# Kernel optimization log

Measured on AMD Instinct MI355X. Metric: run time of the kernel, lower is better.

## Reference

```python
import jax, jax.numpy as jnp
import numpy as np

B, C, T, H, W = 4, 128, 16, 56, 56
NH = 4            # num_heads
HD = C // NH      # head_dim = 32
WT, WH, WW = 4, 7, 7
HID = 4 * C       # mlp hidden
EPS_BN = 1e-5
EPS_LN = 1e-5


def setup_inputs() -> dict:
    key = jax.random.key(0)
    ks = jax.random.split(key, 12)
    s = 0.02
    return {
        "x": jax.random.normal(ks[0], (B, C, T, H, W), dtype=jnp.float32),
        "bn_gamma": jnp.ones((C,), jnp.float32),
        "bn_beta": jnp.zeros((C,), jnp.float32),
        "bn_mean": jax.random.normal(ks[1], (C,), jnp.float32) * 0.1,
        "bn_var": jax.random.uniform(ks[2], (C,), jnp.float32, 0.5, 1.5),
        "qkv_w": jax.random.normal(ks[3], (C, 3 * C), jnp.float32) * s,
        "qkv_b": jnp.zeros((3 * C,), jnp.float32),
        "proj_w": jax.random.normal(ks[4], (C, C), jnp.float32) * s,
        "proj_b": jnp.zeros((C,), jnp.float32),
        "ln_gamma": jnp.ones((C,), jnp.float32),
        "ln_beta": jnp.zeros((C,), jnp.float32),
        "fc1_w": jax.random.normal(ks[5], (C, HID), jnp.float32) * s,
        "fc1_b": jnp.zeros((HID,), jnp.float32),
        "fc2_w": jax.random.normal(ks[6], (HID, C), jnp.float32) * s,
        "fc2_b": jnp.zeros((C,), jnp.float32),
    }


def _window_partition(x):
    # x: (B, C, T, H, W) -> (B*nW, N, C)
    nT, nH, nW = T // WT, H // WH, W // WW
    x = jnp.transpose(x, (0, 2, 3, 4, 1))  # B,T,H,W,C
    x = x.reshape(B, nT, WT, nH, WH, nW, WW, C)
    x = jnp.transpose(x, (0, 1, 3, 5, 2, 4, 6, 7))
    return x.reshape(-1, WT * WH * WW, C)


def _window_reverse(w):
    # w: (B*nW, N, C) -> (B, C, T, H, W)
    nT, nH, nW = T // WT, H // WH, W // WW
    x = w.reshape(B, nT, nH, nW, WT, WH, WW, C)
    x = jnp.transpose(x, (0, 1, 4, 2, 5, 3, 6, 7))
    x = x.reshape(B, T, H, W, C)
    return jnp.transpose(x, (0, 4, 1, 2, 3))


def _forward(x, bn_gamma, bn_beta, bn_mean, bn_var, qkv_w, qkv_b,
             proj_w, proj_b, ln_gamma, ln_beta, fc1_w, fc1_b, fc2_w, fc2_b):
    # --- BN3d (eval mode, running stats) over channel dim ---
    inv = jax.lax.rsqrt(bn_var + EPS_BN)
    bshape = (1, C, 1, 1, 1)
    xn = (x - bn_mean.reshape(bshape)) * (inv * bn_gamma).reshape(bshape) + bn_beta.reshape(bshape)

    # --- windowed MHSA ---
    win = _window_partition(xn)                 # (Bw, N, C)
    Bw, N, _ = win.shape
    qkv = win @ qkv_w + qkv_b                   # (Bw, N, 3C)
    qkv = qkv.reshape(Bw, N, 3, NH, HD)
    q, k, v = [jnp.transpose(qkv[:, :, i], (0, 2, 1, 3)) for i in range(3)]  # (Bw, NH, N, HD)
    scale = 1.0 / np.sqrt(HD).astype(np.float32)
    logits = jnp.einsum('bhnd,bhmd->bhnm', q, k) * scale
    attn = jax.nn.softmax(logits, axis=-1)
    out = jnp.einsum('bhnm,bhmd->bhnd', attn, v)
    out = jnp.transpose(out, (0, 2, 1, 3)).reshape(Bw, N, C)
    out = out @ proj_w + proj_b
    x = x + _window_reverse(out)                # residual

    # --- FFN with LayerNorm on flattened sequence ---
    flat = jnp.transpose(x, (0, 2, 3, 4, 1)).reshape(B, T * H * W, C)
    mu = jnp.mean(flat, axis=-1, keepdims=True)
    var = jnp.var(flat, axis=-1, keepdims=True)
    f = (flat - mu) * jax.lax.rsqrt(var + EPS_LN) * ln_gamma + ln_beta
    f = jax.nn.gelu(f @ fc1_w + fc1_b, approximate=False) @ fc2_w + fc2_b
    flat = flat + f
    return jnp.transpose(flat.reshape(B, T, H, W, C), (0, 4, 1, 2, 3))


def reference(x, bn_gamma, bn_beta, bn_mean, bn_var, qkv_w, qkv_b,
              proj_w, proj_b, ln_gamma, ln_beta, fc1_w, fc1_b, fc2_w, fc2_b):
    return _forward(x, bn_gamma, bn_beta, bn_mean, bn_var, qkv_w, qkv_b,
                    proj_w, proj_b, ln_gamma, ln_beta, fc1_w, fc1_b, fc2_w, fc2_b)
```

## Files before the change

kernel.cpp:

```cpp
#include <hip/hip_runtime.h>
#include <hip/hip_bf16.h>
#include <math.h>


typedef __hip_bfloat16 bf16;
typedef __attribute__((ext_vector_type(8))) short short8;
typedef __attribute__((ext_vector_type(4))) short bhalf4;
typedef __attribute__((ext_vector_type(4))) float f32x4;

__device__ __forceinline__ float b2f(bf16 v) { return __bfloat162float(v); }
__device__ __forceinline__ bf16  f2b(float v) { return __float2bfloat16(v); }

__device__ __forceinline__ float gelu_f(float v) {
    float u = v * 0.70710678118654752f;
    float a = fabsf(u);
    float t = __builtin_amdgcn_rcpf(fmaf(0.3275911f, a, 1.0f));
    float poly = t * fmaf(t, fmaf(t, fmaf(t, fmaf(t, 1.061405429f, -1.453152027f),
                                          1.421413741f), -0.284496736f), 0.254829592f);
    float E = poly * __expf(-a * a);
    float w = (u >= 0.f) ? (2.0f - E) : E;
    return 0.5f * v * w;
}

__global__ __launch_bounds__(256) void k0_prep(
    const float* __restrict__ qkv_w, const float* __restrict__ proj_w,
    const float* __restrict__ w1, const float* __restrict__ w2,
    bf16* __restrict__ qkv_wt, bf16* __restrict__ proj_wt,
    bf16* __restrict__ w1t, bf16* __restrict__ w2t)
{
    int stride = gridDim.x * 256;
    int t0 = blockIdx.x * 256 + threadIdx.x;
    for (int i = t0; i < 384 * 128; i += stride) {
        int j = i >> 7, c = i & 127;
        qkv_wt[i] = f2b(qkv_w[c * 384 + j]);
    }
    for (int i = t0; i < 128 * 128; i += stride) {
        int j = i >> 7, c = i & 127;
        proj_wt[i] = f2b(proj_w[c * 128 + j]);
    }
    for (int i = t0; i < 512 * 128; i += stride) {
        int j = i >> 7, c = i & 127;
        w1t[i] = f2b(w1[c * 512 + j]);
    }
    for (int i = t0; i < 128 * 512; i += stride) {
        int c = i >> 9, j = i & 511;
        w2t[i] = f2b(w2[j * 128 + c]);
    }
}

__global__ __launch_bounds__(256) void k12_bn_qkv(
    const float* __restrict__ x, const float* __restrict__ gamma, const float* __restrict__ beta,
    const float* __restrict__ mean, const float* __restrict__ var,
    const bf16* __restrict__ qkv_wt, const float* __restrict__ qkv_b,
    bf16* __restrict__ Q, bf16* __restrict__ K, bf16* __restrict__ V, int bw0)
{
    __shared__ __align__(16) bf16 sXn[208][136];
    __shared__ __align__(16) bf16 sB[64][136];
    __shared__ float sAc[128], sBc[128];
    int lbw = blockIdx.x;
    int gbw = bw0 + lbw;
    int b   = gbw >> 8;
    int wid = gbw & 255;
    int t0 = (wid >> 6) * 4;
    int h0 = ((wid >> 3) & 7) * 7;
    int w0 = (wid & 7) * 7;
    int tid = threadIdx.x;
    if (tid < 128) {
        float a = gamma[tid] * rsqrtf(var[tid] + 1e-5f);
        sAc[tid] = a;
        sBc[tid] = beta[tid] - mean[tid] * a;
    }
    __syncthreads();
    for (int idx = tid; idx < 128 * 196; idx += 256) {
        int c = idx / 196;
        int n = idx - c * 196;
        int wt = n / 49; int rem = n - wt * 49;
        int wh = rem / 7; int ww = rem - wh * 7;
        int gi = (((b * 128 + c) * 16 + (t0 + wt)) * 56 + (h0 + wh)) * 56 + (w0 + ww);
        sXn[n][c] = f2b(x[gi] * sAc[c] + sBc[c]);
    }
    for (int idx = tid; idx < 12 * 16; idx += 256) {
        int row = 196 + (idx >> 4); int c8 = (idx & 15) * 8;
        *(short8*)&sXn[row][c8] = (short8){0, 0, 0, 0, 0, 0, 0, 0};
    }
    int w = tid >> 6, lane = tid & 63;
    int quad = lane >> 4, l16 = lane & 15;
    const f32x4 zero4 = {0.f, 0.f, 0.f, 0.f};
    for (int jc = 0; jc < 6; ++jc) {
        __syncthreads();
        for (int idx = tid; idx < 1024; idx += 256) {
            int j = idx >> 4; int c8 = (idx & 15) * 8;
            *(short8*)&sB[j][c8] = *(const short8*)&qkv_wt[(long)(jc * 64 + j) * 128 + c8];
        }
        __syncthreads();
        bf16* outw = (jc < 2) ? Q : (jc < 4 ? K : V);
        int jb = (jc & 1) * 64;
        for (int mt = w; mt < 13; mt += 4) {
            f32x4 acc[4];
            #pragma unroll
            for (int nt = 0; nt < 4; ++nt) acc[nt] = zero4;
            #pragma unroll
            for (int kk = 0; kk < 4; ++kk) {
                short8 af = *(const short8*)&sXn[mt * 16 + l16][kk * 32 + quad * 8];
                #pragma unroll
                for (int nt = 0; nt < 4; ++nt) {
                    short8 bfq = *(const short8*)&sB[nt * 16 + l16][kk * 32 + quad * 8];
                    acc[nt] = __builtin_amdgcn_mfma_f32_16x16x32_bf16(af, bfq, acc[nt], 0, 0, 0);
                }
            }
            #pragma unroll
            for (int nt = 0; nt < 4; ++nt) {
                int jcol = jb + nt * 16 + l16;
                int h = jcol >> 5, d = jcol & 31;
                float bias = qkv_b[jc * 64 + nt * 16 + l16];
                bf16* base = outw + ((long)(lbw * 4 + h) * 196) * 32 + d;
                #pragma unroll
                for (int r = 0; r < 4; ++r) {
                    int n = mt * 16 + quad * 4 + r;
                    if (n < 196) base[(long)n * 32] = f2b(acc[nt][r] + bias);
                }
            }
        }
    }
}

__global__ __launch_bounds__(256) void k3_attn(
    const bf16* __restrict__ Q, const bf16* __restrict__ K, const bf16* __restrict__ V,
    bf16* __restrict__ attn_out)
{
    __shared__ __align__(16) bf16 sQ[208][36];
    __shared__ __align__(16) bf16 sK[224][40];
    __shared__ __align__(16) bf16 sVt[32][232];
    __shared__ __align__(16) bf16 sP[4][16][36];
    int bh = blockIdx.x;
    int bw = bh >> 2; int h = bh & 3;
    int tid = threadIdx.x;
    const bf16* qp = Q + (long)bh * 6272;
    const bf16* kp = K + (long)bh * 6272;
    const bf16* vp = V + (long)bh * 6272;
    short8 z8 = {0, 0, 0, 0, 0, 0, 0, 0};
    bhalf4 z4 = {0, 0, 0, 0};
    for (int idx = tid; idx < 784; idx += 256) {
        int row = idx >> 2; int c8 = (idx & 3) * 8;
        short8 qv = *(const short8*)&qp[idx * 8];
        bhalf4 qlo = {qv[0], qv[1], qv[2], qv[3]};
        bhalf4 qhi = {qv[4], qv[5], qv[6], qv[7]};
        *(bhalf4*)&sQ[row][c8]     = qlo;
        *(bhalf4*)&sQ[row][c8 + 4] = qhi;
        *(short8*)&sK[row][c8] = *(const short8*)&kp[idx * 8];
    }
    for (int idx = tid; idx < 48; idx += 256) {
        int row = 196 + (idx >> 2); int c8 = (idx & 3) * 8;
        *(bhalf4*)&sQ[row][c8]     = z4;
        *(bhalf4*)&sQ[row][c8 + 4] = z4;
    }
    for (int idx = tid; idx < 112; idx += 256) {
        *(short8*)&sK[196 + (idx >> 2)][(idx & 3) * 8] = z8;
    }
    for (int idx = tid; idx < 784; idx += 256) {
        int j = idx >> 2; int d0 = (idx & 3) * 8;
        short8 vv = *(const short8*)&vp[j * 32 + d0];
        #pragma unroll
        for (int k = 0; k < 8; ++k) *(short*)&sVt[d0 + k][j] = vv[k];
    }
    for (int idx = tid; idx < 32 * 28; idx += 256) {
        int d = idx / 28; int j = 196 + (idx - d * 28);
        sVt[d][j] = f2b(0.f);
    }
    __syncthreads();
    int w = tid >> 6, lane = tid & 63;
    int quad = lane >> 4, l16 = lane & 15;
    const float scale = 0.17677669529663687f;
    const f32x4 zero4 = {0.f, 0.f, 0.f, 0.f};
    for (int mt = w; mt < 13; mt += 4) {
        bhalf4 qlo = *(const bhalf4*)&sQ[mt * 16 + l16][quad * 8];
        bhalf4 qhi = *(const bhalf4*)&sQ[mt * 16 + l16][quad * 8 + 4];
        short8 qf = {qlo[0], qlo[1], qlo[2], qlo[3], qhi[0], qhi[1], qhi[2], qhi[3]};
        f32x4 oacc0 = zero4, oacc1 = zero4;
        float lsum[4] = {0.f, 0.f, 0.f, 0.f};
        for (int cc = 0; cc < 7; ++cc) {
            #pragma unroll
            for (int t2 = 0; t2 < 2; ++t2) {
                int col0 = cc * 32 + t2 * 16;
                short8 kf = *(const short8*)&sK[col0 + l16][quad * 8];
                f32x4 s = __builtin_amdgcn_mfma_f32_16x16x32_bf16(qf, kf, zero4, 0, 0, 0);
                bool valid = (col0 + l16) < 196;
                #pragma unroll
                for (int r = 0; r < 4; ++r) {
                    float p = valid ? __expf(s[r] * scale) : 0.f;
                    lsum[r] += p;
                    sP[w][quad * 4 + r][t2 * 16 + l16] = f2b(p);
                }
            }
            bhalf4 plo = *(const bhalf4*)&sP[w][l16][quad * 8];
            bhalf4 phi = *(const bhalf4*)&sP[w][l16][quad * 8 + 4];
            short8 pf = {plo[0], plo[1], plo[2], plo[3], phi[0], phi[1], phi[2], phi[3]};
            short8 vf0 = *(const short8*)&sVt[l16][cc * 32 + quad * 8];
            short8 vf1 = *(const short8*)&sVt[16 + l16][cc * 32 + quad * 8];
            oacc0 = __builtin_amdgcn_mfma_f32_16x16x32_bf16(pf, vf0, oacc0, 0, 0, 0);
            oacc1 = __builtin_amdgcn_mfma_f32_16x16x32_bf16(pf, vf1, oacc1, 0, 0, 0);
        }
        #pragma unroll
        for (int off = 1; off < 16; off <<= 1) {
            #pragma unroll
            for (int r = 0; r < 4; ++r) lsum[r] += __shfl_xor(lsum[r], off, 64);
        }
        #pragma unroll
        for (int r = 0; r < 4; ++r) {
            int row = mt * 16 + quad * 4 + r;
            if (row < 196) {
                float inv = 1.0f / lsum[r];
                bf16* op = attn_out + ((long)(bw * 196) + row) * 128 + h * 32;
                op[l16]      = f2b(oacc0[r] * inv);
                op[16 + l16] = f2b(oacc1[r] * inv);
            }
        }
    }
}

__global__ __launch_bounds__(256) void k4_proj(
    const bf16* __restrict__ attn, const bf16* __restrict__ proj_wt, const float* __restrict__ proj_b,
    const float* __restrict__ x, float* __restrict__ y, int bw0)
{
    __shared__ __align__(16) bf16 sA[64][136];
    __shared__ __align__(16) bf16 sB[64][136];
    __shared__ float sC[64][69];
    int t0 = blockIdx.x * 64;
    int j0 = blockIdx.y * 64;
    int tid = threadIdx.x;
    for (int idx = tid; idx < 64 * 16; idx += 256) {
        int i = idx >> 4; int c8 = (idx & 15) * 8;
        *(short8*)&sA[i][c8] = *(const short8*)&attn[(long)(t0 + i) * 128 + c8];
    }
    for (int idx = tid; idx < 64 * 16; idx += 256) {
        int j = idx >> 4; int c8 = (idx & 15) * 8;
        *(short8*)&sB[j][c8] = *(const short8*)&proj_wt[(long)(j0 + j) * 128 + c8];
    }
    __syncthreads();
    int w = tid >> 6, lane = tid & 63;
    int quad = lane >> 4, l16 = lane & 15;
    int w16 = w * 16;
    f32x4 acc[4];
    #pragma unroll
    for (int nt = 0; nt < 4; ++nt) acc[nt] = (f32x4){0.f, 0.f, 0.f, 0.f};
    #pragma unroll
    for (int kk = 0; kk < 4; ++kk) {
        short8 af = *(const short8*)&sA[w16 + l16][kk * 32 + quad * 8];
        #pragma unroll
        for (int nt = 0; nt < 4; ++nt) {
            short8 bfq = *(const short8*)&sB[nt * 16 + l16][kk * 32 + quad * 8];
            acc[nt] = __builtin_amdgcn_mfma_f32_16x16x32_bf16(af, bfq, acc[nt], 0, 0, 0);
        }
    }
    #pragma unroll
    for (int nt = 0; nt < 4; ++nt) {
        int n = nt * 16 + l16;
        float bias = proj_b[j0 + n];
        #pragma unroll
        for (int r = 0; r < 4; ++r) {
            sC[w16 + quad * 4 + r][n] = acc[nt][r] + bias;
        }
    }
    __syncthreads();
    for (int idx = tid; idx < 4096; idx += 256) {
        int j = idx >> 6; int tl = idx & 63;
        int gj = j0 + j;
        int tk = t0 + tl;
        int lbw = tk / 196; int n = tk - lbw * 196;
        int gbw = bw0 + lbw;
        int b = gbw >> 8; int wid = gbw & 255;
        int wt = n / 49; int rem = n - wt * 49;
        int tt = (wid >> 6) * 4 + wt;
        int hh = ((wid >> 3) & 7) * 7 + rem / 7;
        int wcol = (wid & 7) * 7 + (rem - (rem / 7) * 7);
        int thw = (tt * 56 + hh) * 56 + wcol;
        long off = (long)(b * 128 + gj) * 50176 + thw;
        y[off] = sC[tl][j] + x[off];
    }
}

__global__ __launch_bounds__(256, 4) void k5_mlp(
    float* __restrict__ y,
    const float* __restrict__ ln_g, const float* __restrict__ ln_b,
    const bf16* __restrict__ w1t, const float* __restrict__ b1,
    const bf16* __restrict__ w2t, const float* __restrict__ b2)
{
    __shared__ __align__(16) unsigned char Rraw[18944];
    __shared__ __align__(16) bf16 sH[64][36];
    bf16 (*lnT)[136] = (bf16(*)[136])Rraw;
    bf16 (*sW1)[136] = (bf16(*)[136])Rraw;
    bf16 (*sW2)[40]  = (bf16(*)[40])(Rraw + 32 * 136 * 2);
    float* sPa   = (float*)&sH[0][0];
    float* sPb   = sPa + 256;
    float* sMu   = sPb + 256;
    float* sRstd = sMu + 64;

    int tid = threadIdx.x;
    int g0 = blockIdx.x * 64;
    int b = g0 / 50176;
    int thw0 = g0 - b * 50176;
    int tok = tid & 63;
    int cg = tid >> 6;
    int c0 = cg * 32;
    float* yb = y + (long)(b * 128 + c0) * 50176 + thw0 + tok;

    {
        float res[32];
        float s = 0.f, s2 = 0.f;
        #pragma unroll
        for (int k = 0; k < 32; ++k) {
            float v = yb[(long)k * 50176];
            res[k] = v; s += v; s2 += v * v;
        }
        sPa[cg * 64 + tok] = s; sPb[cg * 64 + tok] = s2;
        __syncthreads();
        if (tid < 64) {
            float ss  = sPa[tid] + sPa[64 + tid] + sPa[128 + tid] + sPa[192 + tid];
            float ss2 = sPb[tid] + sPb[64 + tid] + sPb[128 + tid] + sPb[192 + tid];
            float mu = ss * (1.0f / 128.0f);
            float var = ss2 * (1.0f / 128.0f) - mu * mu;
            sMu[tid] = mu;
            sRstd[tid] = rsqrtf(fmaxf(var, 0.f) + 1e-5f);
        }
        __syncthreads();
        float mu = sMu[tok], rstd = sRstd[tok];
        #pragma unroll
        for (int k8 = 0; k8 < 4; ++k8) {
            short8 pk;
            #pragma unroll
            for (int k = 0; k < 8; ++k) {
                int c = c0 + k8 * 8 + k;
                bf16 hv = f2b((res[k8 * 8 + k] - mu) * rstd * ln_g[c] + ln_b[c]);
                pk[k] = *(short*)&hv;
            }
            *(short8*)&lnT[tok][c0 + k8 * 8] = pk;
        }
    }
    __syncthreads();

    int w = tid >> 6, lane = tid & 63;
    int quad = lane >> 4, l16 = lane & 15;
    int w16 = w * 16;
    short8 afr[4];
    #pragma unroll
    for (int kk = 0; kk < 4; ++kk)
        afr[kk] = *(const short8*)&lnT[w16 + l16][kk * 32 + quad * 8];
    __syncthreads();

    int j0i = tid >> 4, c8a = (tid & 15) * 8;
    int ca  = tid >> 2, j8a = (tid & 3) * 8;
    short8 r1a, r1b, r2a, r2b;
    r1a = *(const short8*)&w1t[(long)(0 * 32 + j0i) * 128 + c8a];
    r1b = *(const short8*)&w1t[(long)(0 * 32 + j0i + 16) * 128 + c8a];
    r2a = *(const short8*)&w2t[(long)ca * 512 + 0 * 32 + j8a];
    r2b = *(const short8*)&w2t[(long)(ca + 64) * 512 + 0 * 32 + j8a];
    *(short8*)&sW1[j0i][c8a]      = r1a;
    *(short8*)&sW1[j0i + 16][c8a] = r1b;
    *(short8*)&sW2[ca][j8a]       = r2a;
    *(short8*)&sW2[ca + 64][j8a]  = r2b;
    __syncthreads();

    f32x4 facc[8];
    #pragma unroll
    for (int t = 0; t < 8; ++t) facc[t] = (f32x4){0.f, 0.f, 0.f, 0.f};

    for (int ch = 0; ch < 16; ++ch) {
        if (ch < 15) {
            r1a = *(const short8*)&w1t[(long)((ch + 1) * 32 + j0i) * 128 + c8a];
            r1b = *(const short8*)&w1t[(long)((ch + 1) * 32 + j0i + 16) * 128 + c8a];
            r2a = *(const short8*)&w2t[(long)ca * 512 + (ch + 1) * 32 + j8a];
            r2b = *(const short8*)&w2t[(long)(ca + 64) * 512 + (ch + 1) * 32 + j8a];
        }
        #pragma unroll
        for (int t = 0; t < 2; ++t) {
            f32x4 a = (f32x4){0.f, 0.f, 0.f, 0.f};
            #pragma unroll
            for (int kk = 0; kk < 4; ++kk) {
                short8 bfq = *(const short8*)&sW1[t * 16 + l16][kk * 32 + quad * 8];
                a = __builtin_amdgcn_mfma_f32_16x16x32_bf16(afr[kk], bfq, a, 0, 0, 0);
            }
            float bias = b1[ch * 32 + t * 16 + l16];
            #pragma unroll
            for (int r = 0; r < 4; ++r) {
                sH[w16 + quad * 4 + r][t * 16 + l16] = f2b(gelu_f(a[r] + bias));
            }
        }
        bhalf4 h0 = *(const bhalf4*)&sH[w16 + l16][quad * 8];
        bhalf4 h1 = *(const bhalf4*)&sH[w16 + l16][quad * 8 + 4];
        short8 hf = {h0[0], h0[1], h0[2], h0[3], h1[0], h1[1], h1[2], h1[3]};
        #pragma unroll
        for (int t = 0; t < 8; ++t) {
            short8 wf = *(const short8*)&sW2[t * 16 + l16][quad * 8];
            facc[t] = __builtin_amdgcn_mfma_f32_16x16x32_bf16(hf, wf, facc[t], 0, 0, 0);
        }
        if (ch < 15) {
            __syncthreads();
            *(short8*)&sW1[j0i][c8a]      = r1a;
            *(short8*)&sW1[j0i + 16][c8a] = r1b;
            *(short8*)&sW2[ca][j8a]       = r2a;
            *(short8*)&sW2[ca + 64][j8a]  = r2b;
            __syncthreads();
        }
    }
    __syncthreads();
    bf16 (*sOut)[136] = lnT;
    #pragma unroll
    for (int t = 0; t < 8; ++t) {
        int c = t * 16 + l16;
        float b2v = b2[c];
        #pragma unroll
        for (int r = 0; r < 4; ++r) {
            sOut[w16 + quad * 4 + r][c] = f2b(facc[t][r] + b2v);
        }
    }
    __syncthreads();
    #pragma unroll
    for (int k8 = 0; k8 < 4; ++k8) {
        short8 ov = *(const short8*)&sOut[tok][c0 + k8 * 8];
        #pragma unroll
        for (int k = 0; k < 8; ++k) {
            short sv = ov[k];
            bf16 bv = *(bf16*)&sv;
            long off = (long)(k8 * 8 + k) * 50176;
            yb[off] = yb[off] + b2f(bv);
        }
    }
}

extern "C" void kernel_launch(void* const* d_in, const int* in_sizes, int n_in,
                              void* d_out, int out_size, void* d_ws, size_t ws_size,
                              hipStream_t stream) {
    const float* x      = (const float*)d_in[0];
    const float* bn_g   = (const float*)d_in[1];
    const float* bn_b   = (const float*)d_in[2];
    const float* bn_m   = (const float*)d_in[3];
    const float* bn_v   = (const float*)d_in[4];
    const float* qkv_w  = (const float*)d_in[5];
    const float* qkv_b  = (const float*)d_in[6];
    const float* proj_w = (const float*)d_in[7];
    const float* proj_b = (const float*)d_in[8];
    const float* ln_g   = (const float*)d_in[9];
    const float* ln_b   = (const float*)d_in[10];
    const float* fc1_w  = (const float*)d_in[11];
    const float* fc1_b  = (const float*)d_in[12];
    const float* fc2_w  = (const float*)d_in[13];
    const float* fc2_b  = (const float*)d_in[14];
    float* out = (float*)d_out;

    const size_t WB = 393216;
    char* ws = (char*)d_ws;
    bf16* qkv_wt  = (bf16*)ws;
    bf16* proj_wt = qkv_wt + 384 * 128;
    bf16* w1t     = proj_wt + 128 * 128;
    bf16* w2t     = w1t + 512 * 128;
    char* ws2 = ws + WB;

    int NB = 1;
    while (NB < 64 && (205520896ull / NB + WB) > ws_size) NB *= 2;
    int WPB = 1024 / NB;
    int TPB = WPB * 196;
    size_t seg = (size_t)TPB * 128 * 2;

    bf16* win = (bf16*)(ws2);
    bf16* Qb  = (bf16*)(ws2 + seg);
    bf16* Kb  = (bf16*)(ws2 + 2 * seg);
    bf16* Vb  = (bf16*)(ws2 + 3 * seg);

    k0_prep<<<dim3(192), dim3(256), 0, stream>>>(qkv_w, proj_w, fc1_w, fc2_w,
                                                 qkv_wt, proj_wt, w1t, w2t);
    for (int bi = 0; bi < NB; ++bi) {
        int bw0 = bi * WPB;
        k12_bn_qkv<<<dim3(WPB), dim3(256), 0, stream>>>(x, bn_g, bn_b, bn_m, bn_v,
                                                        qkv_wt, qkv_b, Qb, Kb, Vb, bw0);
        k3_attn<<<dim3(WPB * 4), dim3(256), 0, stream>>>(Qb, Kb, Vb, win);
        k4_proj<<<dim3(TPB / 64, 2), dim3(256), 0, stream>>>(win, proj_wt, proj_b, x, out, bw0);
    }
    k5_mlp<<<dim3(3136), dim3(256), 0, stream>>>(out, ln_g, ln_b, w1t, fc1_b, w2t, fc2_b);
}
```

Baseline: 694.0 us.

## Fuse BN+QKV projection into attention kernel per window-head

Merges the BN/QKV GEMM kernel and the attention kernel into one kernel launched per (window, head). Each block reads x directly from global memory, normalizes it into MFMA fragments in registers, and computes its head's K, V and Q into shared memory and registers. This removes the Q/K/V round trip through global memory and the workspace it needed. In exchange, each of the four head blocks re-reads the whole window's input and recomputes the BN'd activations, reading x with strided, uncoalesced per-channel loads.

Result: slower. 844.6 us (+21.7%).

```diff
diff --git a/kernel.cpp b/kernel.cpp
--- a/kernel.cpp
+++ b/kernel.cpp
@@ -48,171 +48,165 @@
     }
 }
 
-__global__ __launch_bounds__(256) void k12_bn_qkv(
+__global__ __launch_bounds__(256, 3) void k123_attn(
     const float* __restrict__ x, const float* __restrict__ gamma, const float* __restrict__ beta,
     const float* __restrict__ mean, const float* __restrict__ var,
     const bf16* __restrict__ qkv_wt, const float* __restrict__ qkv_b,
-    bf16* __restrict__ Q, bf16* __restrict__ K, bf16* __restrict__ V, int bw0)
+    bf16* __restrict__ attn_out, int bw0)
 {
-    __shared__ __align__(16) bf16 sXn[208][136];
-    __shared__ __align__(16) bf16 sB[64][136];
+    __shared__ __align__(16) bf16 sK[224][40];
+    __shared__ __align__(16) bf16 sVt[32][232];
+    __shared__ __align__(16) bf16 sP[4][16][36];
     __shared__ float sAc[128], sBc[128];
-    int lbw = blockIdx.x;
-    int gbw = bw0 + lbw;
+    int bh = blockIdx.x;
+    int bw = bh >> 2; int h = bh & 3;
+    int gbw = bw0 + bw;
     int b   = gbw >> 8;
     int wid = gbw & 255;
     int t0 = (wid >> 6) * 4;
     int h0 = ((wid >> 3) & 7) * 7;
     int w0 = (wid & 7) * 7;
     int tid = threadIdx.x;
+    short8 z8 = {0, 0, 0, 0, 0, 0, 0, 0};
     if (tid < 128) {
         float a = gamma[tid] * rsqrtf(var[tid] + 1e-5f);
         sAc[tid] = a;
         sBc[tid] = beta[tid] - mean[tid] * a;
     }
-    __syncthreads();
-    for (int idx = tid; idx < 128 * 196; idx += 256) {
-        int c = idx / 196;
-        int n = idx - c * 196;
-        int wt = n / 49; int rem = n - wt * 49;
-        int wh = rem / 7; int ww = rem - wh * 7;
-        int gi = (((b * 128 + c) * 16 + (t0 + wt)) * 56 + (h0 + wh)) * 56 + (w0 + ww);
-        sXn[n][c] = f2b(x[gi] * sAc[c] + sBc[c]);
-    }
-    for (int idx = tid; idx < 12 * 16; idx += 256) {
-        int row = 196 + (idx >> 4); int c8 = (idx & 15) * 8;
-        *(short8*)&sXn[row][c8] = (short8){0, 0, 0, 0, 0, 0, 0, 0};
-    }
+    for (int idx = tid; idx < 80; idx += 256) {
+        int r = 208 + idx / 5; int c8 = (idx % 5) * 8;
+        *(short8*)&sK[r][c8] = z8;
+    }
+    for (int idx = tid; idx < 768; idx += 256) {
+        int d = idx / 24; int j = 208 + (idx % 24);
+        sVt[d][j] = f2b(0.f);
+    }
+    __syncthreads();
+
     int w = tid >> 6, lane = tid & 63;
     int quad = lane >> 4, l16 = lane & 15;
+    const float* xb = x + (long)b * 128 * 50176;
     const f32x4 zero4 = {0.f, 0.f, 0.f, 0.f};
-    for (int jc = 0; jc < 6; ++jc) {
-        __syncthreads();
-        for (int idx = tid; idx < 1024; idx += 256) {
-            int j = idx >> 4; int c8 = (idx & 15) * 8;
-            *(short8*)&sB[j][c8] = *(const short8*)&qkv_wt[(long)(jc * 64 + j) * 128 + c8];
-        }
-        __syncthreads();
-        bf16* outw = (jc < 2) ? Q : (jc < 4 ? K : V);
-        int jb = (jc & 1) * 64;
-        for (int mt = w; mt < 13; mt += 4) {
-            f32x4 acc[4];
-            #pragma unroll
-            for (int nt = 0; nt < 4; ++nt) acc[nt] = zero4;
+    int baseq = h * 32, basek = 128 + h * 32, basev = 256 + h * 32;
+    float bq0 = qkv_b[baseq + l16],  bq1 = qkv_b[baseq + 16 + l16];
+    float bk0 = qkv_b[basek + l16],  bk1 = qkv_b[basek + 16 + l16];
+    float bv0 = qkv_b[basev + l16],  bv1 = qkv_b[basev + 16 + l16];
+
+    short8 qfr[4];
+    #pragma unroll
+    for (int ti = 0; ti < 4; ++ti) {
+        int mt = w + ti * 4;
+        if (mt < 13) {
+            int n = mt * 16 + l16;
+            bool av = n < 196;
+            int nn = av ? n : 0;
+            int wt = nn / 49; int rem = nn - wt * 49;
+            int wh = rem / 7; int ww = rem - wh * 7;
+            long thw = ((long)(t0 + wt) * 56 + (h0 + wh)) * 56 + (w0 + ww);
+            short8 af[4];
             #pragma unroll
             for (int kk = 0; kk < 4; ++kk) {
-                short8 af = *(const short8*)&sXn[mt * 16 + l16][kk * 32 + quad * 8];
                 #pragma unroll
-                for (int nt = 0; nt < 4; ++nt) {
-                    short8 bfq = *(const short8*)&sB[nt * 16 + l16][kk * 32 + quad * 8];
-                    acc[nt] = __builtin_amdgcn_mfma_f32_16x16x32_bf16(af, bfq, acc[nt], 0, 0, 0);
+                for (int k = 0; k < 8; ++k) {
+                    int c = kk * 32 + quad * 8 + k;
+                    float v = xb[(long)c * 50176 + thw];
+                    bf16 bvv = f2b(v * sAc[c] + sBc[c]);
+                    af[kk][k] = av ? *(short*)&bvv : (short)0;
                 }
             }
-            #pragma unroll
-            for (int nt = 0; nt < 4; ++nt) {
-                int jcol = jb + nt * 16 + l16;
-                int h = jcol >> 5, d = jcol & 31;
-                float bias = qkv_b[jc * 64 + nt * 16 + l16];
-                bf16* base = outw + ((long)(lbw * 4 + h) * 196) * 32 + d;
+            f32x4 c0, c1;
+            c0 = zero4; c1 = zero4;
+            #pragma unroll
+            for (int kk = 0; kk < 4; ++kk) {
+                short8 wb0 = *(const short8*)&qkv_wt[(long)(basek + l16) * 128 + kk * 32 + quad * 8];
+                short8 wb1 = *(const short8*)&qkv_wt[(long)(basek + 16 + l16) * 128 + kk * 32 + quad * 8];
+                c0 = __builtin_amdgcn_mfma_f32_16x16x32_bf16(af[kk], wb0, c0, 0, 0, 0);
+                c1 = __builtin_amdgcn_mfma_f32_16x16x32_bf16(af[kk], wb1, c1, 0, 0, 0);
+            }
+            #pragma unroll
+            for (int r = 0; r < 4; ++r) {
+                int row = mt * 16 + quad * 4 + r;
+                sK[row][l16]      = f2b(c0[r] + bk0);
+                sK[row][16 + l16] = f2b(c1[r] + bk1);
+            }
+            c0 = zero4; c1 = zero4;
+            #pragma unroll
+            for (int kk = 0; kk < 4; ++kk) {
+                short8 wb0 = *(const short8*)&qkv_wt[(long)(basev + l16) * 128 + kk * 32 + quad * 8];
+                short8 wb1 = *(const short8*)&qkv_wt[(long)(basev + 16 + l16) * 128 + kk * 32 + quad * 8];
+                c0 = __builtin_amdgcn_mfma_f32_16x16x32_bf16(af[kk], wb0, c0, 0, 0, 0);
+                c1 = __builtin_amdgcn_mfma_f32_16x16x32_bf16(af[kk], wb1, c1, 0, 0, 0);
+            }
+            #pragma unroll
+            for (int r = 0; r < 4; ++r) {
+                int j = mt * 16 + quad * 4 + r;
+                sVt[l16][j]      = f2b(c0[r] + bv0);
+                sVt[16 + l16][j] = f2b(c1[r] + bv1);
+            }
+            c0 = zero4; c1 = zero4;
+            #pragma unroll
+            for (int kk = 0; kk < 4; ++kk) {
+                short8 wb0 = *(const short8*)&qkv_wt[(long)(baseq + l16) * 128 + kk * 32 + quad * 8];
+                short8 wb1 = *(const short8*)&qkv_wt[(long)(baseq + 16 + l16) * 128 + kk * 32 + quad * 8];
+                c0 = __builtin_amdgcn_mfma_f32_16x16x32_bf16(af[kk], wb0, c0, 0, 0, 0);
+                c1 = __builtin_amdgcn_mfma_f32_16x16x32_bf16(af[kk], wb1, c1, 0, 0, 0);
+            }
+            #pragma unroll
+            for (int r = 0; r < 4; ++r) {
+                sP[w][quad * 4 + r][l16]      = f2b(c0[r] + bq0);
+                sP[w][quad * 4 + r][16 + l16] = f2b(c1[r] + bq1);
+            }
+            bhalf4 qlo = *(const bhalf4*)&sP[w][l16][quad * 8];
+            bhalf4 qhi = *(const bhalf4*)&sP[w][l16][quad * 8 + 4];
+            qfr[ti] = (short8){qlo[0], qlo[1], qlo[2], qlo[3], qhi[0], qhi[1], qhi[2], qhi[3]};
+        }
+    }
+    __syncthreads();
+
+    const float scale = 0.17677669529663687f;
+    #pragma unroll
+    for (int ti = 0; ti < 4; ++ti) {
+        int mt = w + ti * 4;
+        if (mt < 13) {
+            short8 qf = qfr[ti];
+            f32x4 oacc0 = zero4, oacc1 = zero4;
+            float lsum[4] = {0.f, 0.f, 0.f, 0.f};
+            for (int cc = 0; cc < 7; ++cc) {
                 #pragma unroll
-                for (int r = 0; r < 4; ++r) {
-                    int n = mt * 16 + quad * 4 + r;
-                    if (n < 196) base[(long)n * 32] = f2b(acc[nt][r] + bias);
+                for (int t2 = 0; t2 < 2; ++t2) {
+                    int col0 = cc * 32 + t2 * 16;
+                    short8 kf = *(const short8*)&sK[col0 + l16][quad * 8];
+                    f32x4 s = __builtin_amdgcn_mfma_f32_16x16x32_bf16(qf, kf, zero4, 0, 0, 0);
+                    bool valid = (col0 + l16) < 196;
+                    #pragma unroll
+                    for (int r = 0; r < 4; ++r) {
+                        float p = valid ? __expf(s[r] * scale) : 0.f;
+                        lsum[r] += p;
+                        sP[w][quad * 4 + r][t2 * 16 + l16] = f2b(p);
+                    }
                 }
-            }
-        }
-    }
-}
-
-__global__ __launch_bounds__(256) void k3_attn(
-    const bf16* __restrict__ Q, const bf16* __restrict__ K, const bf16* __restrict__ V,
-    bf16* __restrict__ attn_out)
-{
-    __shared__ __align__(16) bf16 sQ[208][36];
-    __shared__ __align__(16) bf16 sK[224][40];
-    __shared__ __align__(16) bf16 sVt[32][232];
-    __shared__ __align__(16) bf16 sP[4][16][36];
-    int bh = blockIdx.x;
-    int bw = bh >> 2; int h = bh & 3;
-    int tid = threadIdx.x;
-    const bf16* qp = Q + (long)bh * 6272;
-    const bf16* kp = K + (long)bh * 6272;
-    const bf16* vp = V + (long)bh * 6272;
-    short8 z8 = {0, 0, 0, 0, 0, 0, 0, 0};
-    bhalf4 z4 = {0, 0, 0, 0};
-    for (int idx = tid; idx < 784; idx += 256) {
-        int row = idx >> 2; int c8 = (idx & 3) * 8;
-        short8 qv = *(const short8*)&qp[idx * 8];
-        bhalf4 qlo = {qv[0], qv[1], qv[2], qv[3]};
-        bhalf4 qhi = {qv[4], qv[5], qv[6], qv[7]};
-        *(bhalf4*)&sQ[row][c8]     = qlo;
-        *(bhalf4*)&sQ[row][c8 + 4] = qhi;
-        *(short8*)&sK[row][c8] = *(const short8*)&kp[idx * 8];
-    }
-    for (int idx = tid; idx < 48; idx += 256) {
-        int row = 196 + (idx >> 2); int c8 = (idx & 3) * 8;
-        *(bhalf4*)&sQ[row][c8]     = z4;
-        *(bhalf4*)&sQ[row][c8 + 4] = z4;
-    }
-    for (int idx = tid; idx < 112; idx += 256) {
-        *(short8*)&sK[196 + (idx >> 2)][(idx & 3) * 8] = z8;
-    }
-    for (int idx = tid; idx < 784; idx += 256) {
-        int j = idx >> 2; int d0 = (idx & 3) * 8;
-        short8 vv = *(const short8*)&vp[j * 32 + d0];
-        #pragma unroll
-        for (int k = 0; k < 8; ++k) *(short*)&sVt[d0 + k][j] = vv[k];
-    }
-    for (int idx = tid; idx < 32 * 28; idx += 256) {
-        int d = idx / 28; int j = 196 + (idx - d * 28);
-        sVt[d][j] = f2b(0.f);
-    }
-    __syncthreads();
-    int w = tid >> 6, lane = tid & 63;
-    int quad = lane >> 4, l16 = lane & 15;
-    const float scale = 0.17677669529663687f;
-    const f32x4 zero4 = {0.f, 0.f, 0.f, 0.f};
-    for (int mt = w; mt < 13; mt += 4) {
-        bhalf4 qlo = *(const bhalf4*)&sQ[mt * 16 + l16][quad * 8];
-        bhalf4 qhi = *(const bhalf4*)&sQ[mt * 16 + l16][quad * 8 + 4];
-        short8 qf = {qlo[0], qlo[1], qlo[2], qlo[3], qhi[0], qhi[1], qhi[2], qhi[3]};
-        f32x4 oacc0 = zero4, oacc1 = zero4;
-        float lsum[4] = {0.f, 0.f, 0.f, 0.f};
-        for (int cc = 0; cc < 7; ++cc) {
-            #pragma unroll
-            for (int t2 = 0; t2 < 2; ++t2) {
-                int col0 = cc * 32 + t2 * 16;
-                short8 kf = *(const short8*)&sK[col0 + l16][quad * 8];
-                f32x4 s = __builtin_amdgcn_mfma_f32_16x16x32_bf16(qf, kf, zero4, 0, 0, 0);
-                bool valid = (col0 + l16) < 196;
+                bhalf4 plo = *(const bhalf4*)&sP[w][l16][quad * 8];
+                bhalf4 phi = *(const bhalf4*)&sP[w][l16][quad * 8 + 4];
+                short8 pf = {plo[0], plo[1], plo[2], plo[3], phi[0], phi[1], phi[2], phi[3]};
+                short8 vf0 = *(const short8*)&sVt[l16][cc * 32 + quad * 8];
+                short8 vf1 = *(const short8*)&sVt[16 + l16][cc * 32 + quad * 8];
+                oacc0 = __builtin_amdgcn_mfma_f32_16x16x32_bf16(pf, vf0, oacc0, 0, 0, 0);
+                oacc1 = __builtin_amdgcn_mfma_f32_16x16x32_bf16(pf, vf1, oacc1, 0, 0, 0);
+            }
+            #pragma unroll
+            for (int off = 1; off < 16; off <<= 1) {
                 #pragma unroll
-                for (int r = 0; r < 4; ++r) {
-                    float p = valid ? __expf(s[r] * scale) : 0.f;
-                    lsum[r] += p;
-                    sP[w][quad * 4 + r][t2 * 16 + l16] = f2b(p);
+                for (int r = 0; r < 4; ++r) lsum[r] += __shfl_xor(lsum[r], off, 64);
+            }
+            #pragma unroll
+            for (int r = 0; r < 4; ++r) {
+                int row = mt * 16 + quad * 4 + r;
+                if (row < 196) {
+                    float inv = 1.0f / lsum[r];
+                    bf16* op = attn_out + ((long)(bw * 196) + row) * 128 + h * 32;
+                    op[l16]      = f2b(oacc0[r] * inv);
+                    op[16 + l16] = f2b(oacc1[r] * inv);
                 }
-            }
-            bhalf4 plo = *(const bhalf4*)&sP[w][l16][quad * 8];
-            bhalf4 phi = *(const bhalf4*)&sP[w][l16][quad * 8 + 4];
-            short8 pf = {plo[0], plo[1], plo[2], plo[3], phi[0], phi[1], phi[2], phi[3]};
-            short8 vf0 = *(const short8*)&sVt[l16][cc * 32 + quad * 8];
-            short8 vf1 = *(const short8*)&sVt[16 + l16][cc * 32 + quad * 8];
-            oacc0 = __builtin_amdgcn_mfma_f32_16x16x32_bf16(pf, vf0, oacc0, 0, 0, 0);
-            oacc1 = __builtin_amdgcn_mfma_f32_16x16x32_bf16(pf, vf1, oacc1, 0, 0, 0);
-        }
-        #pragma unroll
-        for (int off = 1; off < 16; off <<= 1) {
-            #pragma unroll
-            for (int r = 0; r < 4; ++r) lsum[r] += __shfl_xor(lsum[r], off, 64);
-        }
-        #pragma unroll
-        for (int r = 0; r < 4; ++r) {
-            int row = mt * 16 + quad * 4 + r;
-            if (row < 196) {
-                float inv = 1.0f / lsum[r];
-                bf16* op = attn_out + ((long)(bw * 196) + row) * 128 + h * 32;
-                op[l16]      = f2b(oacc0[r] * inv);
-                op[16 + l16] = f2b(oacc1[r] * inv);
             }
         }
     }
@@ -456,24 +450,19 @@
     char* ws2 = ws + WB;
 
     int NB = 1;
-    while (NB < 64 && (205520896ull / NB + WB) > ws_size) NB *= 2;
+    while (NB < 64 && (51380224ull / NB + WB) > ws_size) NB *= 2;
     int WPB = 1024 / NB;
     int TPB = WPB * 196;
-    size_t seg = (size_t)TPB * 128 * 2;
-
-    bf16* win = (bf16*)(ws2);
-    bf16* Qb  = (bf16*)(ws2 + seg);
-    bf16* Kb  = (bf16*)(ws2 + 2 * seg);
-    bf16* Vb  = (bf16*)(ws2 + 3 * seg);
+
+    bf16* attn = (bf16*)(ws2);
 
     k0_prep<<<dim3(192), dim3(256), 0, stream>>>(qkv_w, proj_w, fc1_w, fc2_w,
                                                  qkv_wt, proj_wt, w1t, w2t);
     for (int bi = 0; bi < NB; ++bi) {
         int bw0 = bi * WPB;
-        k12_bn_qkv<<<dim3(WPB), dim3(256), 0, stream>>>(x, bn_g, bn_b, bn_m, bn_v,
-                                                        qkv_wt, qkv_b, Qb, Kb, Vb, bw0);
-        k3_attn<<<dim3(WPB * 4), dim3(256), 0, stream>>>(Qb, Kb, Vb, win);
-        k4_proj<<<dim3(TPB / 64, 2), dim3(256), 0, stream>>>(win, proj_wt, proj_b, x, out, bw0);
+        k123_attn<<<dim3(WPB * 4), dim3(256), 0, stream>>>(x, bn_g, bn_b, bn_m, bn_v,
+                                                           qkv_wt, qkv_b, attn, bw0);
+        k4_proj<<<dim3(TPB / 64, 2), dim3(256), 0, stream>>>(attn, proj_wt, proj_b, x, out, bw0);
     }
     k5_mlp<<<dim3(3136), dim3(256), 0, stream>>>(out, ln_g, ln_b, w1t, fc1_b, w2t, fc2_b);
 }
```

## Fuse output projection, residual, LayerNorm and MLP into one kernel

Applied to the files above, without the earlier changes.

Merges the projection kernel and the MLP kernel so each block gathers 64 tokens in spatial order from the window-ordered attention output. It computes the projection plus residual and keeps the result in registers for LayerNorm and the FFN. This removes the fp32 write and re-read of the intermediate activation through global memory and drops one launch. In exchange it uses more shared memory, lowers occupancy, adds a gathered row load, and caps the batch split at 16. It also assumes every chunk of window tokens lines up with whole spatial rows.

Result: faster. 564.9 us (-18.6%).

```diff
diff --git a/kernel.cpp b/kernel.cpp
--- a/kernel.cpp
+++ b/kernel.cpp
@@ -218,129 +218,126 @@
     }
 }
 
-__global__ __launch_bounds__(256) void k4_proj(
+__global__ __launch_bounds__(256, 3) void k45_proj_mlp(
     const bf16* __restrict__ attn, const bf16* __restrict__ proj_wt, const float* __restrict__ proj_b,
-    const float* __restrict__ x, float* __restrict__ y, int bw0)
-{
-    __shared__ __align__(16) bf16 sA[64][136];
-    __shared__ __align__(16) bf16 sB[64][136];
-    __shared__ float sC[64][69];
-    int t0 = blockIdx.x * 64;
-    int j0 = blockIdx.y * 64;
-    int tid = threadIdx.x;
-    for (int idx = tid; idx < 64 * 16; idx += 256) {
-        int i = idx >> 4; int c8 = (idx & 15) * 8;
-        *(short8*)&sA[i][c8] = *(const short8*)&attn[(long)(t0 + i) * 128 + c8];
-    }
-    for (int idx = tid; idx < 64 * 16; idx += 256) {
-        int j = idx >> 4; int c8 = (idx & 15) * 8;
-        *(short8*)&sB[j][c8] = *(const short8*)&proj_wt[(long)(j0 + j) * 128 + c8];
-    }
-    __syncthreads();
-    int w = tid >> 6, lane = tid & 63;
-    int quad = lane >> 4, l16 = lane & 15;
-    int w16 = w * 16;
-    f32x4 acc[4];
-    #pragma unroll
-    for (int nt = 0; nt < 4; ++nt) acc[nt] = (f32x4){0.f, 0.f, 0.f, 0.f};
-    #pragma unroll
-    for (int kk = 0; kk < 4; ++kk) {
-        short8 af = *(const short8*)&sA[w16 + l16][kk * 32 + quad * 8];
-        #pragma unroll
-        for (int nt = 0; nt < 4; ++nt) {
-            short8 bfq = *(const short8*)&sB[nt * 16 + l16][kk * 32 + quad * 8];
-            acc[nt] = __builtin_amdgcn_mfma_f32_16x16x32_bf16(af, bfq, acc[nt], 0, 0, 0);
-        }
-    }
-    #pragma unroll
-    for (int nt = 0; nt < 4; ++nt) {
-        int n = nt * 16 + l16;
-        float bias = proj_b[j0 + n];
-        #pragma unroll
-        for (int r = 0; r < 4; ++r) {
-            sC[w16 + quad * 4 + r][n] = acc[nt][r] + bias;
-        }
-    }
-    __syncthreads();
-    for (int idx = tid; idx < 4096; idx += 256) {
-        int j = idx >> 6; int tl = idx & 63;
-        int gj = j0 + j;
-        int tk = t0 + tl;
-        int lbw = tk / 196; int n = tk - lbw * 196;
-        int gbw = bw0 + lbw;
-        int b = gbw >> 8; int wid = gbw & 255;
-        int wt = n / 49; int rem = n - wt * 49;
-        int tt = (wid >> 6) * 4 + wt;
-        int hh = ((wid >> 3) & 7) * 7 + rem / 7;
-        int wcol = (wid & 7) * 7 + (rem - (rem / 7) * 7);
-        int thw = (tt * 56 + hh) * 56 + wcol;
-        long off = (long)(b * 128 + gj) * 50176 + thw;
-        y[off] = sC[tl][j] + x[off];
-    }
-}
-
-__global__ __launch_bounds__(256, 4) void k5_mlp(
-    float* __restrict__ y,
+    const float* __restrict__ x, float* __restrict__ y,
     const float* __restrict__ ln_g, const float* __restrict__ ln_b,
     const bf16* __restrict__ w1t, const float* __restrict__ b1,
-    const bf16* __restrict__ w2t, const float* __restrict__ b2)
+    const bf16* __restrict__ w2t, const float* __restrict__ b2, int bw0)
 {
-    __shared__ __align__(16) unsigned char Rraw[18944];
-    __shared__ __align__(16) bf16 sH[64][36];
-    bf16 (*lnT)[136] = (bf16(*)[136])Rraw;
-    bf16 (*sW1)[136] = (bf16(*)[136])Rraw;
-    bf16 (*sW2)[40]  = (bf16(*)[40])(Rraw + 32 * 136 * 2);
-    float* sPa   = (float*)&sH[0][0];
+    __shared__ __align__(16) unsigned char pool[52480];
+    bf16 (*sA)[136]  = (bf16(*)[136])pool;
+    bf16 (*lnT)[136] = (bf16(*)[136])pool;
+    bf16 (*sB)[136]  = (bf16(*)[136])(pool + 17408);
+    bf16 (*sW1)[136] = (bf16(*)[136])(pool + 17408);
+    bf16 (*sW2)[40]  = (bf16(*)[40]) (pool + 17408 + 8704);
+    float (*sCf)[69] = (float(*)[69])(pool + 34816);
+    bf16 (*sH)[36]   = (bf16(*)[36]) (pool + 36352);
+    float* sPa   = (float*)(pool + 17408);
     float* sPb   = sPa + 256;
     float* sMu   = sPb + 256;
     float* sRstd = sMu + 64;
+    int*   sRow  = (int*)(pool + 40960);
 
     int tid = threadIdx.x;
-    int g0 = blockIdx.x * 64;
-    int b = g0 / 50176;
-    int thw0 = g0 - b * 50176;
+    long g0 = (long)bw0 * 196 + (long)blockIdx.x * 64;
+    int b = (int)(g0 / 50176);
+    int thw0 = (int)(g0 - (long)b * 50176);
     int tok = tid & 63;
     int cg = tid >> 6;
-    int c0 = cg * 32;
-    float* yb = y + (long)(b * 128 + c0) * 50176 + thw0 + tok;
-
-    {
-        float res[32];
-        float s = 0.f, s2 = 0.f;
-        #pragma unroll
-        for (int k = 0; k < 32; ++k) {
-            float v = yb[(long)k * 50176];
-            res[k] = v; s += v; s2 += v * v;
-        }
-        sPa[cg * 64 + tok] = s; sPb[cg * 64 + tok] = s2;
-        __syncthreads();
-        if (tid < 64) {
-            float ss  = sPa[tid] + sPa[64 + tid] + sPa[128 + tid] + sPa[192 + tid];
-            float ss2 = sPb[tid] + sPb[64 + tid] + sPb[128 + tid] + sPb[192 + tid];
-            float mu = ss * (1.0f / 128.0f);
-            float var = ss2 * (1.0f / 128.0f) - mu * mu;
-            sMu[tid] = mu;
-            sRstd[tid] = rsqrtf(fmaxf(var, 0.f) + 1e-5f);
-        }
-        __syncthreads();
-        float mu = sMu[tok], rstd = sRstd[tok];
-        #pragma unroll
-        for (int k8 = 0; k8 < 4; ++k8) {
-            short8 pk;
-            #pragma unroll
-            for (int k = 0; k < 8; ++k) {
-                int c = c0 + k8 * 8 + k;
-                bf16 hv = f2b((res[k8 * 8 + k] - mu) * rstd * ln_g[c] + ln_b[c]);
-                pk[k] = *(short*)&hv;
-            }
-            *(short8*)&lnT[tok][c0 + k8 * 8] = pk;
-        }
-    }
-    __syncthreads();
-
-    int w = tid >> 6, lane = tid & 63;
+    int w = cg, lane = tid & 63;
     int quad = lane >> 4, l16 = lane & 15;
     int w16 = w * 16;
+
+    if (tid < 64) {
+        int thw = thw0 + tid;
+        int t = thw / 3136; int r2 = thw - t * 3136;
+        int hh = r2 / 56;   int ww = r2 - hh * 56;
+        int wid = (t >> 2) * 64 + (hh / 7) * 8 + (ww / 7);
+        int n = (t & 3) * 49 + (hh % 7) * 7 + (ww % 7);
+        sRow[tid] = (b * 256 + wid - bw0) * 196 + n;
+    }
+    __syncthreads();
+    for (int idx = tid; idx < 1024; idx += 256) {
+        int m = idx >> 4; int c8 = (idx & 15) * 8;
+        *(short8*)&sA[m][c8] = *(const short8*)&attn[(long)sRow[m] * 128 + c8];
+    }
+    for (int idx = tid; idx < 1024; idx += 256) {
+        int j = idx >> 4; int c8 = (idx & 15) * 8;
+        *(short8*)&sB[j][c8] = *(const short8*)&proj_wt[(long)j * 128 + c8];
+    }
+    __syncthreads();
+
+    float res[32];
+    float s = 0.f, s2 = 0.f;
+    const f32x4 zero4 = {0.f, 0.f, 0.f, 0.f};
+    for (int jc = 0; jc < 2; ++jc) {
+        if (jc == 1) {
+            __syncthreads();
+            for (int idx = tid; idx < 1024; idx += 256) {
+                int j = idx >> 4; int c8 = (idx & 15) * 8;
+                *(short8*)&sB[j][c8] = *(const short8*)&proj_wt[(long)(64 + j) * 128 + c8];
+            }
+            __syncthreads();
+        }
+        f32x4 acc[4];
+        #pragma unroll
+        for (int nt = 0; nt < 4; ++nt) acc[nt] = zero4;
+        #pragma unroll
+        for (int kk = 0; kk < 4; ++kk) {
+            short8 af = *(const short8*)&sA[w16 + l16][kk * 32 + quad * 8];
+            #pragma unroll
+            for (int nt = 0; nt < 4; ++nt) {
+                short8 bfq = *(const short8*)&sB[nt * 16 + l16][kk * 32 + quad * 8];
+                acc[nt] = __builtin_amdgcn_mfma_f32_16x16x32_bf16(af, bfq, acc[nt], 0, 0, 0);
+            }
+        }
+        #pragma unroll
+        for (int nt = 0; nt < 4; ++nt) {
+            int n = nt * 16 + l16;
+            float bias = proj_b[jc * 64 + n];
+            #pragma unroll
+            for (int r = 0; r < 4; ++r) sCf[w16 + quad * 4 + r][n] = acc[nt][r] + bias;
+        }
+        __syncthreads();
+        #pragma unroll
+        for (int k = 0; k < 16; ++k) {
+            int cl = cg * 16 + k;
+            int c = jc * 64 + cl;
+            float v = sCf[tok][cl] + x[(long)(b * 128 + c) * 50176 + thw0 + tok];
+            res[jc * 16 + k] = v; s += v; s2 += v * v;
+        }
+    }
+    __syncthreads();
+    sPa[cg * 64 + tok] = s; sPb[cg * 64 + tok] = s2;
+    __syncthreads();
+    if (tid < 64) {
+        float ss  = sPa[tid] + sPa[64 + tid] + sPa[128 + tid] + sPa[192 + tid];
+        float ss2 = sPb[tid] + sPb[64 + tid] + sPb[128 + tid] + sPb[192 + tid];
+        float mu = ss * (1.0f / 128.0f);
+        float var = ss2 * (1.0f / 128.0f) - mu * mu;
+        sMu[tid] = mu;
+        sRstd[tid] = rsqrtf(fmaxf(var, 0.f) + 1e-5f);
+    }
+    __syncthreads();
+    {
+        float mu = sMu[tok], rstd = sRstd[tok];
+        #pragma unroll
+        for (int jc = 0; jc < 2; ++jc) {
+            #pragma unroll
+            for (int k8 = 0; k8 < 2; ++k8) {
+                short8 pk;
+                #pragma unroll
+                for (int k = 0; k < 8; ++k) {
+                    int c = jc * 64 + cg * 16 + k8 * 8 + k;
+                    bf16 hv = f2b((res[jc * 16 + k8 * 8 + k] - mu) * rstd * ln_g[c] + ln_b[c]);
+                    pk[k] = *(short*)&hv;
+                }
+                *(short8*)&lnT[tok][jc * 64 + cg * 16 + k8 * 8] = pk;
+            }
+        }
+    }
+    __syncthreads();
     short8 afr[4];
     #pragma unroll
     for (int kk = 0; kk < 4; ++kk)
@@ -350,10 +347,10 @@
     int j0i = tid >> 4, c8a = (tid & 15) * 8;
     int ca  = tid >> 2, j8a = (tid & 3) * 8;
     short8 r1a, r1b, r2a, r2b;
-    r1a = *(const short8*)&w1t[(long)(0 * 32 + j0i) * 128 + c8a];
-    r1b = *(const short8*)&w1t[(long)(0 * 32 + j0i + 16) * 128 + c8a];
-    r2a = *(const short8*)&w2t[(long)ca * 512 + 0 * 32 + j8a];
-    r2b = *(const short8*)&w2t[(long)(ca + 64) * 512 + 0 * 32 + j8a];
+    r1a = *(const short8*)&w1t[(long)j0i * 128 + c8a];
+    r1b = *(const short8*)&w1t[(long)(j0i + 16) * 128 + c8a];
+    r2a = *(const short8*)&w2t[(long)ca * 512 + j8a];
+    r2b = *(const short8*)&w2t[(long)(ca + 64) * 512 + j8a];
     *(short8*)&sW1[j0i][c8a]      = r1a;
     *(short8*)&sW1[j0i + 16][c8a] = r1b;
     *(short8*)&sW2[ca][j8a]       = r2a;
@@ -415,14 +412,17 @@
     }
     __syncthreads();
     #pragma unroll
-    for (int k8 = 0; k8 < 4; ++k8) {
-        short8 ov = *(const short8*)&sOut[tok][c0 + k8 * 8];
-        #pragma unroll
-        for (int k = 0; k < 8; ++k) {
-            short sv = ov[k];
-            bf16 bv = *(bf16*)&sv;
-            long off = (long)(k8 * 8 + k) * 50176;
-            yb[off] = yb[off] + b2f(bv);
+    for (int jc = 0; jc < 2; ++jc) {
+        #pragma unroll
+        for (int k8 = 0; k8 < 2; ++k8) {
+            short8 ov = *(const short8*)&sOut[tok][jc * 64 + cg * 16 + k8 * 8];
+            #pragma unroll
+            for (int k = 0; k < 8; ++k) {
+                short sv = ov[k];
+                bf16 bv = *(bf16*)&sv;
+                int c = jc * 64 + cg * 16 + k8 * 8 + k;
+                y[(long)(b * 128 + c) * 50176 + thw0 + tok] = res[jc * 16 + k8 * 8 + k] + b2f(bv);
+            }
         }
     }
 }
@@ -456,15 +456,15 @@
     char* ws2 = ws + WB;
 
     int NB = 1;
-    while (NB < 64 && (205520896ull / NB + WB) > ws_size) NB *= 2;
+    while (NB < 16 && (205520896ull / NB + WB) > ws_size) NB *= 2;
     int WPB = 1024 / NB;
     int TPB = WPB * 196;
     size_t seg = (size_t)TPB * 128 * 2;
 
-    bf16* win = (bf16*)(ws2);
-    bf16* Qb  = (bf16*)(ws2 + seg);
-    bf16* Kb  = (bf16*)(ws2 + 2 * seg);
-    bf16* Vb  = (bf16*)(ws2 + 3 * seg);
+    bf16* attn = (bf16*)(ws2);
+    bf16* Qb   = (bf16*)(ws2 + seg);
+    bf16* Kb   = (bf16*)(ws2 + 2 * seg);
+    bf16* Vb   = (bf16*)(ws2 + 3 * seg);
 
     k0_prep<<<dim3(192), dim3(256), 0, stream>>>(qkv_w, proj_w, fc1_w, fc2_w,
                                                  qkv_wt, proj_wt, w1t, w2t);
@@ -472,8 +472,8 @@
         int bw0 = bi * WPB;
         k12_bn_qkv<<<dim3(WPB), dim3(256), 0, stream>>>(x, bn_g, bn_b, bn_m, bn_v,
                                                         qkv_wt, qkv_b, Qb, Kb, Vb, bw0);
-        k3_attn<<<dim3(WPB * 4), dim3(256), 0, stream>>>(Qb, Kb, Vb, win);
-        k4_proj<<<dim3(TPB / 64, 2), dim3(256), 0, stream>>>(win, proj_wt, proj_b, x, out, bw0);
-    }
-    k5_mlp<<<dim3(3136), dim3(256), 0, stream>>>(out, ln_g, ln_b, w1t, fc1_b, w2t, fc2_b);
-}
+        k3_attn<<<dim3(WPB * 4), dim3(256), 0, stream>>>(Qb, Kb, Vb, attn);
+        k45_proj_mlp<<<dim3(TPB / 64), dim3(256), 0, stream>>>(attn, proj_wt, proj_b, x, out,
+                                                               ln_g, ln_b, w1t, fc1_b, w2t, fc2_b, bw0);
+    }
+}
```
